# Optimization experiments

Measured on AMD Instinct MI355X. Metric: run time of the kernel, lower is better.

The kernel has to match this reference:

```python
import jax, jax.numpy as jnp
import numpy as np

EMB = 128
SQRT_EMB = 128 ** 0.5
LOGIT_CLIP = 10.0


def setup_inputs() -> dict:
    key = jax.random.key(0)
    ks = jax.random.split(key, 10)
    B, N, M, D = 128, 512, 512, EMB
    s = 1.0 / np.sqrt(D)
    return {
        "encoded_last_node": jax.random.normal(ks[0], (B, N, D), jnp.float32),
        "load": jax.random.uniform(ks[1], (B, N), jnp.float32),
        "cur_dist": jax.random.uniform(ks[2], (B, N, M), jnp.float32),
        "log_scale": jnp.ones((), jnp.float32),
        "ninf_mask": jnp.zeros((B, N, M), jnp.float32),
        "encoded_nodes": jax.random.normal(ks[3], (B, M, D), jnp.float32),
        "Wq_last": jax.random.normal(ks[4], (D, D + 1), jnp.float32) * s,
        "Wk": jax.random.normal(ks[5], (D, D), jnp.float32) * s,
        "Wv": jax.random.normal(ks[6], (D, D), jnp.float32) * s,
        "alpha1": jnp.ones((1,), jnp.float32),
        "alpha2": jnp.ones((1,), jnp.float32),
    }


def reference(encoded_last_node, load, cur_dist, log_scale, ninf_mask,
              encoded_nodes, Wq_last, Wk, Wv, alpha1, alpha2):
    # set_kv
    k = jnp.einsum('bmd,ed->bme', encoded_nodes, Wk)   # (B,M,D)
    v = jnp.einsum('bmd,ed->bme', encoded_nodes, Wv)   # (B,M,D)
    # query from last node + load
    input_cat = jnp.concatenate([encoded_last_node, load[:, :, None]], axis=2)  # (B,N,D+1)
    q = jnp.einsum('bnc,ec->bne', input_cat, Wq_last)  # (B,N,D)
    # AAFM: exp-bias linear attention with sigmoid gate
    adaptation_bias = -alpha1[0] * log_scale * cur_dist + ninf_mask  # (B,N,M)
    eb = jnp.exp(adaptation_bias)
    ek = jnp.exp(k)
    num = jnp.einsum('bnm,bmd->bnd', eb, ek * v)
    den = jnp.einsum('bnm,bmd->bnd', eb, ek)
    weighted = jnp.nan_to_num(num / den)  # mirrors torch nan_to_num correction
    aafm_out = jax.nn.sigmoid(q) * weighted  # (B,N,D)
    # single-head decode score against encoder embeddings
    score = jnp.einsum('bnd,bmd->bnm', aafm_out, encoded_nodes)
    score_scaled = score / SQRT_EMB - alpha2[0] * log_scale * cur_dist
    score_masked = LOGIT_CLIP * jnp.tanh(score_scaled) + ninf_mask
    probs = jax.nn.softmax(score_masked, axis=-1)
    return probs
```

## Files before the change

### kernel.cpp

```cpp
#include <hip/hip_runtime.h>
#include <math.h>

#define B 128
#define N 512
#define M 512
#define D 128

typedef __attribute__((ext_vector_type(8))) short s16x8;
typedef __attribute__((ext_vector_type(4))) short s16x4;
typedef __attribute__((ext_vector_type(4))) float f32x4;

#define MFMA16(a, b, c) __builtin_amdgcn_mfma_f32_16x16x32_bf16(a, b, c, 0, 0, 0)

#define FENCE()   asm volatile("" ::: "memory")
#define VMCNT4()  asm volatile("s_waitcnt vmcnt(4)" ::: "memory")
#define VMCNT8()  asm volatile("s_waitcnt vmcnt(8)" ::: "memory")
#define VMCNT12() asm volatile("s_waitcnt vmcnt(12)" ::: "memory")
#define VMCNT20() asm volatile("s_waitcnt vmcnt(20)" ::: "memory")
#define LGKMCNT0() asm volatile("s_waitcnt lgkmcnt(0)" ::: "memory")
#define SCHEDBAR() __builtin_amdgcn_sched_barrier(0)

__device__ __forceinline__ void gload16(const void* g, void* l) {
    __builtin_amdgcn_global_load_lds(
        (const __attribute__((address_space(1))) unsigned int*)g,
        (__attribute__((address_space(3))) unsigned int*)l, 16, 0, 0);
}

__device__ __forceinline__ float fast_tanh(float x) {
    x = fminf(fmaxf(x, -15.f), 15.f);
    float E = __expf(2.f * x);
    return 1.f - 2.f / (E + 1.f);
}

__device__ __forceinline__ unsigned short bf16rne(float x) {
    unsigned u = __float_as_uint(x);
    return (unsigned short)((u + 0x7FFF + ((u >> 16) & 1)) >> 16);
}

__device__ __forceinline__ void fsplit(float x, short& h, short& l) {
    unsigned u = __float_as_uint(x);
    h = (short)(u >> 16);
    float fh = __uint_as_float(u & 0xffff0000u);
    l = (short)(__float_as_uint(x - fh) >> 16);
}

__device__ __forceinline__ void fsplit8(float4 x0, float4 x1, s16x8& h, s16x8& l) {
    short a, b;
    fsplit(x0.x, a, b); h[0] = a; l[0] = b;
    fsplit(x0.y, a, b); h[1] = a; l[1] = b;
    fsplit(x0.z, a, b); h[2] = a; l[2] = b;
    fsplit(x0.w, a, b); h[3] = a; l[3] = b;
    fsplit(x1.x, a, b); h[4] = a; l[4] = b;
    fsplit(x1.y, a, b); h[5] = a; l[5] = b;
    fsplit(x1.z, a, b); h[6] = a; l[6] = b;
    fsplit(x1.w, a, b); h[7] = a; l[7] = b;
}

__device__ __forceinline__ void ebpack(float4 c0, float4 c1, float4 f0, float4 f1,
                                       float a1ls, s16x8& a) {
    a[0] = (short)bf16rne(__expf(fmaf(-a1ls, c0.x, f0.x)));
    a[1] = (short)bf16rne(__expf(fmaf(-a1ls, c0.y, f0.y)));
    a[2] = (short)bf16rne(__expf(fmaf(-a1ls, c0.z, f0.z)));
    a[3] = (short)bf16rne(__expf(fmaf(-a1ls, c0.w, f0.w)));
    a[4] = (short)bf16rne(__expf(fmaf(-a1ls, c1.x, f1.x)));
    a[5] = (short)bf16rne(__expf(fmaf(-a1ls, c1.y, f1.y)));
    a[6] = (short)bf16rne(__expf(fmaf(-a1ls, c1.z, f1.z)));
    a[7] = (short)bf16rne(__expf(fmaf(-a1ls, c1.w, f1.w)));
}

__global__ void k_prep_w(const float* __restrict__ Wk, const float* __restrict__ Wv,
                         const float* __restrict__ Wq,
                         unsigned short* __restrict__ Wk_hi, unsigned short* __restrict__ Wk_lo,
                         unsigned short* __restrict__ Wv_hi, unsigned short* __restrict__ Wv_lo,
                         unsigned short* __restrict__ Wq_hi, unsigned short* __restrict__ Wq_lo) {
    int i = blockIdx.x * 256 + threadIdx.x;
    short h, l;
    if (i < 16384) {
        fsplit(Wk[i], h, l); Wk_hi[i] = (unsigned short)h; Wk_lo[i] = (unsigned short)l;
    } else if (i < 32768) {
        int j = i - 16384;
        fsplit(Wv[j], h, l); Wv_hi[j] = (unsigned short)h; Wv_lo[j] = (unsigned short)l;
    } else {
        int j = i - 32768; int e = j >> 7, d = j & 127;
        fsplit(Wq[e * 129 + d], h, l); Wq_hi[j] = (unsigned short)h; Wq_lo[j] = (unsigned short)l;
    }
}

__global__ __launch_bounds__(256) void k_kv(const float* __restrict__ enc,
        const unsigned short* __restrict__ Wk_hi, const unsigned short* __restrict__ Wk_lo,
        const unsigned short* __restrict__ Wv_hi, const unsigned short* __restrict__ Wv_lo,
        unsigned short* __restrict__ EKb, unsigned short* __restrict__ EKVb) {
    int b = blockIdx.y;
    int wave = threadIdx.x >> 6, lane = threadIdx.x & 63;
    int row = lane & 15, kg = lane >> 4;
    int m0 = blockIdx.x * 64 + wave * 16;
    f32x4 acc[16];
#pragma unroll
    for (int i = 0; i < 16; i++) acc[i] = (f32x4)0.f;
    const float* ap = enc + ((size_t)b * M + m0 + row) * D + kg * 8;
#pragma unroll
    for (int ks = 0; ks < 4; ks++) {
        float4 x0 = *(const float4*)(ap + ks * 32);
        float4 x1 = *(const float4*)(ap + ks * 32 + 4);
        s16x8 ah, al;
        fsplit8(x0, x1, ah, al);
        int wb = ks * 32 + kg * 8;
#pragma unroll
        for (int ct = 0; ct < 8; ct++) {
            int e = ct * 16 + row;
            s16x8 bh = *(const s16x8*)(Wk_hi + e * D + wb);
            s16x8 bl = *(const s16x8*)(Wk_lo + e * D + wb);
            acc[ct] = MFMA16(ah, bh, acc[ct]);
            acc[ct] = MFMA16(al, bh, acc[ct]);
            acc[ct] = MFMA16(ah, bl, acc[ct]);
            bh = *(const s16x8*)(Wv_hi + e * D + wb);
            bl = *(const s16x8*)(Wv_lo + e * D + wb);
            acc[8 + ct] = MFMA16(ah, bh, acc[8 + ct]);
            acc[8 + ct] = MFMA16(al, bh, acc[8 + ct]);
            acc[8 + ct] = MFMA16(ah, bl, acc[8 + ct]);
        }
    }
#pragma unroll
    for (int ct = 0; ct < 8; ct++) {
        int e = ct * 16 + row;
        s16x4 kb, vb;
#pragma unroll
        for (int r = 0; r < 4; r++) {
            float ek = __expf(acc[ct][r]);
            float ev = ek * acc[8 + ct][r];
            kb[r] = (short)bf16rne(ek);
            vb[r] = (short)bf16rne(ev);
        }
        int m = m0 + kg * 4;
        int chunk = (m & 31) >> 3;
        int p = chunk ^ (e & 3);
        size_t o = ((size_t)b * D + e) * M + (size_t)(m & ~31) + p * 8 + (m & 7);
        *(s16x4*)(EKb + o) = kb;
        *(s16x4*)(EKVb + o) = vb;
    }
}

__global__ void k_encpack(const float* __restrict__ enc, unsigned short* __restrict__ Eb) {
    size_t i = (size_t)blockIdx.x * 256 + threadIdx.x;
    size_t bm = i >> 4;
    int c = (int)(i & 15);
    int m = (int)(bm & 511);
    int p = c ^ (m & 7);
    const float* src = enc + bm * 128 + c * 8;
    float4 x0 = *(const float4*)(src);
    float4 x1 = *(const float4*)(src + 4);
    s16x8 v;
    v[0] = (short)bf16rne(x0.x); v[1] = (short)bf16rne(x0.y);
    v[2] = (short)bf16rne(x0.z); v[3] = (short)bf16rne(x0.w);
    v[4] = (short)bf16rne(x1.x); v[5] = (short)bf16rne(x1.y);
    v[6] = (short)bf16rne(x1.z); v[7] = (short)bf16rne(x1.w);
    *(s16x8*)(Eb + bm * 128 + p * 8) = v;
}

__global__ __launch_bounds__(256, 3) void k_fused(
        const float* __restrict__ encl, const float* __restrict__ loadv,
        const float* __restrict__ Wq,
        const unsigned short* __restrict__ Wq_hi, const unsigned short* __restrict__ Wq_lo,
        const float* __restrict__ cd, const float* __restrict__ ninf,
        const unsigned short* __restrict__ EKVb, const unsigned short* __restrict__ EKb,
        const unsigned short* __restrict__ Eb,
        const float* __restrict__ a1p, const float* __restrict__ a2p,
        const float* __restrict__ lsp, float* __restrict__ out) {
    int o = blockIdx.x;
    int xcd = o & 7, j = o >> 3;
    int b = ((j >> 4) << 3) + xcd;
    int nb = j & 15;
    int n0 = nb * 32;
    int w = threadIdx.x >> 6, lane = threadIdx.x & 63;
    int row = lane & 15, kg = lane >> 4;
    __shared__ __align__(16) char lds[32768];
    __shared__ float redm[32][4], reds[32][4];
    float a1ls = a1p[0] * lsp[0];
    float a2ls = a2p[0] * lsp[0];
    const float invs = 0.08838834764831845f;
    char* wb = lds + w * 8192;

    f32x4 sqa[2][2];
#pragma unroll
    for (int s = 0; s < 2; s++)
#pragma unroll
        for (int ct = 0; ct < 2; ct++) sqa[s][ct] = (f32x4)0.f;
#pragma unroll
    for (int s = 0; s < 2; s++) {
        const float* ap = encl + ((size_t)b * N + n0 + s * 16 + row) * D + kg * 8;
#pragma unroll
        for (int ks = 0; ks < 4; ks++) {
            float4 x0 = *(const float4*)(ap + ks * 32);
            float4 x1 = *(const float4*)(ap + ks * 32 + 4);
            s16x8 ah, al;
            fsplit8(x0, x1, ah, al);
            int wqo = ks * 32 + kg * 8;
#pragma unroll
            for (int ct = 0; ct < 2; ct++) {
                int e = w * 32 + ct * 16 + row;
                s16x8 bh = *(const s16x8*)(Wq_hi + e * D + wqo);
                s16x8 bl = *(const s16x8*)(Wq_lo + e * D + wqo);
                sqa[s][ct] = MFMA16(ah, bh, sqa[s][ct]);
                sqa[s][ct] = MFMA16(al, bh, sqa[s][ct]);
                sqa[s][ct] = MFMA16(ah, bl, sqa[s][ct]);
            }
        }
    }
    float sqv[2][2][4];
#pragma unroll
    for (int s = 0; s < 2; s++)
#pragma unroll
        for (int ct = 0; ct < 2; ct++) {
            int e = w * 32 + ct * 16 + row;
            float wcol = Wq[e * 129 + 128];
#pragma unroll
            for (int r = 0; r < 4; r++) {
                int n = n0 + s * 16 + kg * 4 + r;
                float q = sqa[s][ct][r] + loadv[(size_t)b * N + n] * wcol;
                sqv[s][ct][r] = 1.f / (1.f + __expf(-q));
            }
        }
    FENCE();

    f32x4 accN[2][2], accD[2][2];
#pragma unroll
    for (int s = 0; s < 2; s++)
#pragma unroll
        for (int i = 0; i < 2; i++) { accN[s][i] = (f32x4)0.f; accD[s][i] = (f32x4)0.f; }
    const char* gEKV = (const char*)EKVb + (size_t)b * D * M * 2;
    const char* gEK  = (const char*)EKb  + (size_t)b * D * M * 2;
    const float* cdp0 = cd + ((size_t)b * N + n0 + row) * M + kg * 8;
    const float* nfp0 = ninf + ((size_t)b * N + n0 + row) * M + kg * 8;
    const float* cdp1 = cdp0 + (size_t)16 * M;
    const float* nfp1 = nfp0 + (size_t)16 * M;

#define STAGE_B(bufptr, mt)                                                      \
    _Pragma("unroll")                                                            \
    for (int jv = 0; jv < 4; jv++) {                                             \
        int arr = jv >> 1;                                                       \
        int rem = (jv & 1) * 64 + lane;                                          \
        const char* gb = arr ? gEK : gEKV;                                       \
        gload16(gb + (size_t)(w * 32 + (rem >> 2)) * 1024 + (size_t)(mt) * 64 +  \
                    (rem & 3) * 16,                                              \
                (char*)(bufptr) + arr * 2048 + rem * 16);                        \
    }

    float4 Ac[2][2][2], Af[2][2][2];
#define LOAD_A(p, mt)                                                            \
    Ac[p][0][0] = *(const float4*)(cdp0 + (mt) * 32);                            \
    Ac[p][0][1] = *(const float4*)(cdp0 + (mt) * 32 + 4);                        \
    Af[p][0][0] = *(const float4*)(nfp0 + (mt) * 32);                            \
    Af[p][0][1] = *(const float4*)(nfp0 + (mt) * 32 + 4);                        \
    Ac[p][1][0] = *(const float4*)(cdp1 + (mt) * 32);                            \
    Ac[p][1][1] = *(const float4*)(cdp1 + (mt) * 32 + 4);                        \
    Af[p][1][0] = *(const float4*)(nfp1 + (mt) * 32);                            \
    Af[p][1][1] = *(const float4*)(nfp1 + (mt) * 32 + 4);

    LOAD_A(0, 0) FENCE();
    STAGE_B(wb, 0) FENCE();
    LOAD_A(1, 1) FENCE();
    STAGE_B(wb + 4096, 1) FENCE();

    int rbB = row * 64 + ((kg ^ (row & 3)) << 4);
#pragma unroll
    for (int mt = 0; mt < 16; mt++) {
        if (mt < 2) { VMCNT12(); } else if (mt < 15) { VMCNT20(); } else { VMCNT8(); }
        SCHEDBAR();
        int p = mt & 1;
        s16x8 a0, a1;
        ebpack(Ac[p][0][0], Ac[p][0][1], Af[p][0][0], Af[p][0][1], a1ls, a0);
        ebpack(Ac[p][1][0], Ac[p][1][1], Af[p][1][0], Af[p][1][1], a1ls, a1);
        const char* L = wb + p * 4096;
#pragma unroll
        for (int ct = 0; ct < 2; ct++) {
            int ro = ct * 1024 + rbB;
            s16x8 bv = *(const s16x8*)(L + ro);
            s16x8 bk = *(const s16x8*)(L + 2048 + ro);
            accN[0][ct] = MFMA16(a0, bv, accN[0][ct]);
            accN[1][ct] = MFMA16(a1, bv, accN[1][ct]);
            accD[0][ct] = MFMA16(a0, bk, accD[0][ct]);
            accD[1][ct] = MFMA16(a1, bk, accD[1][ct]);
        }
        if (mt <= 13) {
            LGKMCNT0();
            SCHEDBAR();
            STAGE_B(wb + p * 4096, mt + 2) FENCE();
            LOAD_A(p, mt + 2) FENCE();
        }
    }

    __syncthreads();
    float* af = (float*)lds;
#pragma unroll
    for (int s = 0; s < 2; s++)
#pragma unroll
        for (int ct = 0; ct < 2; ct++) {
            int e = w * 32 + ct * 16 + row;
#pragma unroll
            for (int r = 0; r < 4; r++) {
                int nl = s * 16 + kg * 4 + r;
                float num = accN[s][ct][r], den = accD[s][ct][r];
                float ww = (den != 0.f) ? num / den : 0.f;
                float aafm = sqv[s][ct][r] * ww;
                unsigned u = __float_as_uint(aafm);
                unsigned hi = u >> 16;
                float fh = __uint_as_float(u & 0xffff0000u);
                unsigned lo = __float_as_uint(aafm - fh) >> 16;
                af[nl * 128 + e] = __uint_as_float(hi | (lo << 16));
            }
        }
    __syncthreads();
    s16x8 ah[2][4], al[2][4];
#pragma unroll
    for (int s = 0; s < 2; s++)
#pragma unroll
        for (int es = 0; es < 4; es++) {
            const float* src = af + (s * 16 + row) * 128 + es * 32 + kg * 8;
            float4 w0 = *(const float4*)(src);
            float4 w1 = *(const float4*)(src + 4);
            unsigned u;
            u = __float_as_uint(w0.x); ah[s][es][0] = (short)(u & 0xffff); al[s][es][0] = (short)(u >> 16);
            u = __float_as_uint(w0.y); ah[s][es][1] = (short)(u & 0xffff); al[s][es][1] = (short)(u >> 16);
            u = __float_as_uint(w0.z); ah[s][es][2] = (short)(u & 0xffff); al[s][es][2] = (short)(u >> 16);
            u = __float_as_uint(w0.w); ah[s][es][3] = (short)(u & 0xffff); al[s][es][3] = (short)(u >> 16);
            u = __float_as_uint(w1.x); ah[s][es][4] = (short)(u & 0xffff); al[s][es][4] = (short)(u >> 16);
            u = __float_as_uint(w1.y); ah[s][es][5] = (short)(u & 0xffff); al[s][es][5] = (short)(u >> 16);
            u = __float_as_uint(w1.z); ah[s][es][6] = (short)(u & 0xffff); al[s][es][6] = (short)(u >> 16);
            u = __float_as_uint(w1.w); ah[s][es][7] = (short)(u & 0xffff); al[s][es][7] = (short)(u >> 16);
        }
    __syncthreads();
    FENCE();

    f32x4 acc[2][8];
#pragma unroll
    for (int s = 0; s < 2; s++)
#pragma unroll
        for (int p = 0; p < 8; p++) acc[s][p] = (f32x4)0.f;
    const char* gEb = (const char*)Eb + (size_t)b * M * 256;

#define STAGE_D(bufptr, p)                                                       \
    _Pragma("unroll")                                                            \
    for (int jv = 0; jv < 4; jv++) {                                             \
        int id = jv * 64 + lane;                                                 \
        gload16(gEb + (size_t)(w * 128 + (p) * 16 + (id >> 4)) * 256 + (id & 15) * 16, \
                (char*)(bufptr) + id * 16);                                      \
    }

    STAGE_D(wb, 0) FENCE();
    STAGE_D(wb + 4096, 1) FENCE();

#pragma unroll
    for (int p = 0; p < 8; p++) {
        if (p == 0) { VMCNT4(); } else if (p < 7) { VMCNT12(); } else { VMCNT8(); }
        SCHEDBAR();
        float cdv[2][4], nfv[2][4];
#pragma unroll
        for (int s = 0; s < 2; s++)
#pragma unroll
            for (int r = 0; r < 4; r++) {
                size_t idx = ((size_t)b * N + n0 + s * 16 + kg * 4 + r) * M
                           + (size_t)w * 128 + (size_t)p * 16 + row;
                cdv[s][r] = cd[idx];
                nfv[s][r] = ninf[idx];
            }
        FENCE();
        const char* L = wb + (p & 1) * 4096;
        int sw = row & 7;
#pragma unroll
        for (int es = 0; es < 4; es++) {
            int ph = (4 * es + kg) ^ sw;
            s16x8 bb = *(const s16x8*)(L + row * 256 + ph * 16);
            acc[0][p] = MFMA16(ah[0][es], bb, acc[0][p]);
            acc[0][p] = MFMA16(al[0][es], bb, acc[0][p]);
            acc[1][p] = MFMA16(ah[1][es], bb, acc[1][p]);
            acc[1][p] = MFMA16(al[1][es], bb, acc[1][p]);
        }
        if (p <= 5) {
            LGKMCNT0();
            SCHEDBAR();
            STAGE_D(wb + (p & 1) * 4096, p + 2) FENCE();
        }
#pragma unroll
        for (int s = 0; s < 2; s++)
#pragma unroll
            for (int r = 0; r < 4; r++) {
                acc[s][p][r] = 10.f * fast_tanh(fmaf(acc[s][p][r], invs, -a2ls * cdv[s][r]))
                             + nfv[s][r];
            }
    }

    float mx[2][4], sm[2][4];
#pragma unroll
    for (int s = 0; s < 2; s++)
#pragma unroll
        for (int r = 0; r < 4; r++) {
            float m = acc[s][0][r];
#pragma unroll
            for (int p = 1; p < 8; p++) m = fmaxf(m, acc[s][p][r]);
#pragma unroll
            for (int sh = 1; sh < 16; sh <<= 1) m = fmaxf(m, __shfl_xor(m, sh, 64));
            mx[s][r] = m;
        }
    if (row == 0) {
#pragma unroll
        for (int s = 0; s < 2; s++)
#pragma unroll
            for (int r = 0; r < 4; r++) redm[s * 16 + kg * 4 + r][w] = mx[s][r];
    }
    __syncthreads();
#pragma unroll
    for (int s = 0; s < 2; s++)
#pragma unroll
        for (int r = 0; r < 4; r++) {
            int nl = s * 16 + kg * 4 + r;
            float m = fmaxf(fmaxf(redm[nl][0], redm[nl][1]),
                            fmaxf(redm[nl][2], redm[nl][3]));
            float sum = 0.f;
#pragma unroll
            for (int p = 0; p < 8; p++) {
                float e = __expf(acc[s][p][r] - m);
                acc[s][p][r] = e;
                sum += e;
            }
#pragma unroll
            for (int sh = 1; sh < 16; sh <<= 1) sum += __shfl_xor(sum, sh, 64);
            sm[s][r] = sum;
        }
    if (row == 0) {
#pragma unroll
        for (int s = 0; s < 2; s++)
#pragma unroll
            for (int r = 0; r < 4; r++) reds[s * 16 + kg * 4 + r][w] = sm[s][r];
    }
    __syncthreads();
#pragma unroll
    for (int s = 0; s < 2; s++)
#pragma unroll
        for (int r = 0; r < 4; r++) {
            int nl = s * 16 + kg * 4 + r;
            float inv = 1.f / (reds[nl][0] + reds[nl][1] + reds[nl][2] + reds[nl][3]);
            size_t ro = ((size_t)b * N + n0 + nl) * M + (size_t)w * 128 + row;
#pragma unroll
            for (int p = 0; p < 8; p++) {
                out[ro + p * 16] = acc[s][p][r] * inv;
            }
        }
}

extern "C" void kernel_launch(void* const* d_in, const int* in_sizes, int n_in,
                              void* d_out, int out_size, void* d_ws, size_t ws_size,
                              hipStream_t stream) {
    const float* encl  = (const float*)d_in[0];
    const float* loadv = (const float*)d_in[1];
    const float* cdist = (const float*)d_in[2];
    const float* ls    = (const float*)d_in[3];
    const float* ninf  = (const float*)d_in[4];
    const float* enc   = (const float*)d_in[5];
    const float* Wq    = (const float*)d_in[6];
    const float* Wk    = (const float*)d_in[7];
    const float* Wv    = (const float*)d_in[8];
    const float* a1    = (const float*)d_in[9];
    const float* a2    = (const float*)d_in[10];
    char* ws = (char*)d_ws;
    unsigned short* EKb     = (unsigned short*)(ws);
    unsigned short* EKVb    = (unsigned short*)(ws + 16777216);
    unsigned short* Eb      = (unsigned short*)(ws + 33554432);
    unsigned short* Wk_hi   = (unsigned short*)(ws + 50331648);
    unsigned short* Wk_lo   = (unsigned short*)(ws + 50331648 + 32768);
    unsigned short* Wv_hi   = (unsigned short*)(ws + 50331648 + 65536);
    unsigned short* Wv_lo   = (unsigned short*)(ws + 50331648 + 98304);
    unsigned short* Wq_hi   = (unsigned short*)(ws + 50331648 + 131072);
    unsigned short* Wq_lo   = (unsigned short*)(ws + 50331648 + 163840);
    float* out = (float*)d_out;

    k_prep_w<<<192, 256, 0, stream>>>(Wk, Wv, Wq, Wk_hi, Wk_lo, Wv_hi, Wv_lo, Wq_hi, Wq_lo);
    k_kv<<<dim3(8, 128), 256, 0, stream>>>(enc, Wk_hi, Wk_lo, Wv_hi, Wv_lo, EKb, EKVb);
    k_encpack<<<4096, 256, 0, stream>>>(enc, Eb);
    k_fused<<<2048, 256, 0, stream>>>(encl, loadv, Wq, Wq_hi, Wq_lo,
                                      cdist, ninf, EKVb, EKb, Eb,
                                      a1, a2, ls, out);
}
```

Measured before the change: 350.9 us.

## Use single bf16 aafm operand in score GEMM, raise occupancy, alias reduction buffers

The score GEMM previously split aafm_out into hi/lo bf16 halves and issued two MFMAs per step. It now rounds to a single bf16 value, halving that GEMM's MFMAs and the A-fragment registers. The freed registers allow launch bounds of 5 waves per SIMD instead of 3. The softmax reduction arrays now alias the shared LDS buffer, with an extra barrier added. The vmcnt waits are loosened to keep more loads in flight. The cost is lower precision of the score before tanh and softmax.

```diff
diff --git a/kernel.cpp b/kernel.cpp
--- a/kernel.cpp
+++ b/kernel.cpp
@@ -16,6 +16,7 @@
 #define VMCNT4()  asm volatile("s_waitcnt vmcnt(4)" ::: "memory")
 #define VMCNT8()  asm volatile("s_waitcnt vmcnt(8)" ::: "memory")
 #define VMCNT12() asm volatile("s_waitcnt vmcnt(12)" ::: "memory")
+#define VMCNT16() asm volatile("s_waitcnt vmcnt(16)" ::: "memory")
 #define VMCNT20() asm volatile("s_waitcnt vmcnt(20)" ::: "memory")
 #define LGKMCNT0() asm volatile("s_waitcnt lgkmcnt(0)" ::: "memory")
 #define SCHEDBAR() __builtin_amdgcn_sched_barrier(0)
@@ -157,7 +158,7 @@
     *(s16x8*)(Eb + bm * 128 + p * 8) = v;
 }
 
-__global__ __launch_bounds__(256, 3) void k_fused(
+__global__ __launch_bounds__(256, 5) void k_fused(
         const float* __restrict__ encl, const float* __restrict__ loadv,
         const float* __restrict__ Wq,
         const unsigned short* __restrict__ Wq_hi, const unsigned short* __restrict__ Wq_lo,
@@ -174,7 +175,8 @@
     int w = threadIdx.x >> 6, lane = threadIdx.x & 63;
     int row = lane & 15, kg = lane >> 4;
     __shared__ __align__(16) char lds[32768];
-    __shared__ float redm[32][4], reds[32][4];
+    float* redm = (float*)lds;
+    float* reds = (float*)(lds + 512);
     float a1ls = a1p[0] * lsp[0];
     float a2ls = a2p[0] * lsp[0];
     const float invs = 0.08838834764831845f;
@@ -290,7 +292,7 @@
     }
 
     __syncthreads();
-    float* af = (float*)lds;
+    unsigned short* af = (unsigned short*)lds;
 #pragma unroll
     for (int s = 0; s < 2; s++)
 #pragma unroll
@@ -301,33 +303,16 @@
                 int nl = s * 16 + kg * 4 + r;
                 float num = accN[s][ct][r], den = accD[s][ct][r];
                 float ww = (den != 0.f) ? num / den : 0.f;
-                float aafm = sqv[s][ct][r] * ww;
-                unsigned u = __float_as_uint(aafm);
-                unsigned hi = u >> 16;
-                float fh = __uint_as_float(u & 0xffff0000u);
-                unsigned lo = __float_as_uint(aafm - fh) >> 16;
-                af[nl * 128 + e] = __uint_as_float(hi | (lo << 16));
-            }
-        }
-    __syncthreads();
-    s16x8 ah[2][4], al[2][4];
-#pragma unroll
-    for (int s = 0; s < 2; s++)
-#pragma unroll
-        for (int es = 0; es < 4; es++) {
-            const float* src = af + (s * 16 + row) * 128 + es * 32 + kg * 8;
-            float4 w0 = *(const float4*)(src);
-            float4 w1 = *(const float4*)(src + 4);
-            unsigned u;
-            u = __float_as_uint(w0.x); ah[s][es][0] = (short)(u & 0xffff); al[s][es][0] = (short)(u >> 16);
-            u = __float_as_uint(w0.y); ah[s][es][1] = (short)(u & 0xffff); al[s][es][1] = (short)(u >> 16);
-            u = __float_as_uint(w0.z); ah[s][es][2] = (short)(u & 0xffff); al[s][es][2] = (short)(u >> 16);
-            u = __float_as_uint(w0.w); ah[s][es][3] = (short)(u & 0xffff); al[s][es][3] = (short)(u >> 16);
-            u = __float_as_uint(w1.x); ah[s][es][4] = (short)(u & 0xffff); al[s][es][4] = (short)(u >> 16);
-            u = __float_as_uint(w1.y); ah[s][es][5] = (short)(u & 0xffff); al[s][es][5] = (short)(u >> 16);
-            u = __float_as_uint(w1.z); ah[s][es][6] = (short)(u & 0xffff); al[s][es][6] = (short)(u >> 16);
-            u = __float_as_uint(w1.w); ah[s][es][7] = (short)(u & 0xffff); al[s][es][7] = (short)(u >> 16);
-        }
+                af[nl * 128 + e] = bf16rne(sqv[s][ct][r] * ww);
+            }
+        }
+    __syncthreads();
+    s16x8 afr[2][4];
+#pragma unroll
+    for (int s = 0; s < 2; s++)
+#pragma unroll
+        for (int es = 0; es < 4; es++)
+            afr[s][es] = *(const s16x8*)(af + (s * 16 + row) * 128 + es * 32 + kg * 8);
     __syncthreads();
     FENCE();
 
@@ -351,7 +336,7 @@
 
 #pragma unroll
     for (int p = 0; p < 8; p++) {
-        if (p == 0) { VMCNT4(); } else if (p < 7) { VMCNT12(); } else { VMCNT8(); }
+        if (p == 0) { VMCNT4(); } else if (p < 7) { VMCNT20(); } else { VMCNT16(); }
         SCHEDBAR();
         float cdv[2][4], nfv[2][4];
 #pragma unroll
@@ -370,10 +355,8 @@
         for (int es = 0; es < 4; es++) {
             int ph = (4 * es + kg) ^ sw;
             s16x8 bb = *(const s16x8*)(L + row * 256 + ph * 16);
-            acc[0][p] = MFMA16(ah[0][es], bb, acc[0][p]);
-            acc[0][p] = MFMA16(al[0][es], bb, acc[0][p]);
-            acc[1][p] = MFMA16(ah[1][es], bb, acc[1][p]);
-            acc[1][p] = MFMA16(al[1][es], bb, acc[1][p]);
+            acc[0][p] = MFMA16(afr[0][es], bb, acc[0][p]);
+            acc[1][p] = MFMA16(afr[1][es], bb, acc[1][p]);
         }
         if (p <= 5) {
             LGKMCNT0();
@@ -389,6 +372,7 @@
             }
     }
 
+    __syncthreads();
     float mx[2][4], sm[2][4];
 #pragma unroll
     for (int s = 0; s < 2; s++)
@@ -405,7 +389,7 @@
 #pragma unroll
         for (int s = 0; s < 2; s++)
 #pragma unroll
-            for (int r = 0; r < 4; r++) redm[s * 16 + kg * 4 + r][w] = mx[s][r];
+            for (int r = 0; r < 4; r++) redm[(s * 16 + kg * 4 + r) * 4 + w] = mx[s][r];
     }
     __syncthreads();
 #pragma unroll
@@ -413,8 +397,8 @@
 #pragma unroll
         for (int r = 0; r < 4; r++) {
             int nl = s * 16 + kg * 4 + r;
-            float m = fmaxf(fmaxf(redm[nl][0], redm[nl][1]),
-                            fmaxf(redm[nl][2], redm[nl][3]));
+            float m = fmaxf(fmaxf(redm[nl * 4 + 0], redm[nl * 4 + 1]),
+                            fmaxf(redm[nl * 4 + 2], redm[nl * 4 + 3]));
             float sum = 0.f;
 #pragma unroll
             for (int p = 0; p < 8; p++) {
@@ -430,7 +414,7 @@
 #pragma unroll
         for (int s = 0; s < 2; s++)
 #pragma unroll
-            for (int r = 0; r < 4; r++) reds[s * 16 + kg * 4 + r][w] = sm[s][r];
+            for (int r = 0; r < 4; r++) reds[(s * 16 + kg * 4 + r) * 4 + w] = sm[s][r];
     }
     __syncthreads();
 #pragma unroll
@@ -438,7 +422,8 @@
 #pragma unroll
         for (int r = 0; r < 4; r++) {
             int nl = s * 16 + kg * 4 + r;
-            float inv = 1.f / (reds[nl][0] + reds[nl][1] + reds[nl][2] + reds[nl][3]);
+            float inv = 1.f / (reds[nl * 4 + 0] + reds[nl * 4 + 1]
+                             + reds[nl * 4 + 2] + reds[nl * 4 + 3]);
             size_t ro = ((size_t)b * N + n0 + nl) * M + (size_t)w * 128 + row;
 #pragma unroll
             for (int p = 0; p < 8; p++) {
```

Measured after the change: 756.5 us. 116% more time.
